# Kernel tuning notes

Hardware: AMD Instinct MI355X
Metric: run time of the kernel (lower is better)

Reference implementation:

```python
import jax, jax.numpy as jnp
import numpy as np

N, E, D, R = 50000, 600000, 128, 8


def rgcn_conv(x, ei, et, W, root, bias):
    # PyG RGCNConv with aggr='mean', root_weight=True, bias=True.
    src, dst = ei[0], ei[1]
    # per-relation transform of all node features: [N, R, D]
    xw = jnp.einsum('nd,rde->nre', x, W)
    msg = xw[src, et]                      # [E, D] gather per edge
    seg = dst * R + et                     # segment per (node, relation)
    summed = jax.ops.segment_sum(msg, seg, num_segments=N * R)
    cnt = jax.ops.segment_sum(jnp.ones((msg.shape[0],), x.dtype), seg,
                              num_segments=N * R)
    mean = summed / jnp.maximum(cnt, 1.0)[:, None]
    agg = mean.reshape(N, R, D).sum(axis=1)  # sum over relations
    return agg + x @ root + bias


def setup_inputs() -> dict:
    key = jax.random.key(0)
    ks = jax.random.split(key, 9)
    s = 1.0 / np.sqrt(D)
    x = jax.random.normal(ks[0], (N, D), jnp.float32)
    ei = jax.random.randint(ks[1], (2, E), 0, N, jnp.int32)
    et = jax.random.randint(ks[2], (E,), 0, R, jnp.int32)
    W1 = jax.random.normal(ks[3], (R, D, D), jnp.float32) * s
    root1 = jax.random.normal(ks[4], (D, D), jnp.float32) * s
    b1 = jnp.zeros((D,), jnp.float32)
    W2 = jax.random.normal(ks[5], (R, D, D), jnp.float32) * s
    root2 = jax.random.normal(ks[6], (D, D), jnp.float32) * s
    b2 = jnp.zeros((D,), jnp.float32)
    rel_emb = jax.random.normal(ks[7], (R, D), jnp.float32)
    return {"x": x, "ei": ei, "et": et, "W1": W1, "root1": root1, "b1": b1,
            "W2": W2, "root2": root2, "b2": b2, "rel_emb": rel_emb}


def reference(x, ei, et, W1, root1, b1, W2, root2, b2, rel_emb):
    h = jax.nn.relu(rgcn_conv(x, ei, et, W1, root1, b1))
    h = jax.nn.relu(rgcn_conv(h, ei, et, W2, root2, b2))
    return (h, rel_emb)
```

## Files before the change

kernel.cpp:

```cpp
#include <hip/hip_runtime.h>
#include <stdint.h>

#define N_NODES 50000
#define N_EDGES 600000
#define N_REL   8
#define KDIM    1152
#define KA      1024
#define NPAD    50048
#define RCAP    16
#define ZROW    N_NODES

typedef short v8s __attribute__((ext_vector_type(8)));
typedef float v4f __attribute__((ext_vector_type(4)));
typedef float v2f __attribute__((ext_vector_type(2)));
typedef unsigned short u16;
typedef unsigned int   u32;
typedef __attribute__((address_space(1))) const u32 gas_u32;
typedef __attribute__((address_space(3))) u32 las_u32;

__device__ __forceinline__ float bf2f(u16 u) {
    union { u32 i; float f; } t; t.i = ((u32)u) << 16; return t.f;
}
__device__ __forceinline__ u16 f2bf(float f) {
    union { float f; u32 i; } t; t.f = f;
    u32 lsb = (t.i >> 16) & 1u;
    t.i += 0x7fffu + lsb;
    return (u16)(t.i >> 16);
}
__device__ __forceinline__ v2f bfpair(u32 g) {
    union { u32 i; float f; } a, b;
    a.i = g << 16; b.i = g & 0xffff0000u;
    return (v2f){a.f, b.f};
}
__device__ __forceinline__ float load_f(const void* p, int i, int fl) {
    return fl ? bf2f(((const u16*)p)[i]) : ((const float*)p)[i];
}
__device__ __forceinline__ int wave_detect(const u32* __restrict__ x32) {
    u32 w = x32[threadIdx.x & 63];
    u32 e = (w >> 7) & 0xffu;
    unsigned long long m = __ballot(e >= 112u && e < 144u);
    return __popcll(m) >= 32;
}

#define B_CF    2344
#define B_CONV  (B_CF + 3125)
#define B_PREPW (B_CONV + 1153)
#define B_RELEMB (B_PREPW + 4)
__global__ void k_prep(const void* __restrict__ x, const int* __restrict__ ei,
                       const int* __restrict__ et,
                       const void* __restrict__ W1, const void* __restrict__ r1,
                       const void* __restrict__ b1, const void* __restrict__ W2,
                       const void* __restrict__ r2, const void* __restrict__ b2,
                       const void* __restrict__ rel_emb,
                       u16* __restrict__ xc, u16* __restrict__ Wbig,
                       u16* __restrict__ bc, int* __restrict__ cnt,
                       u16* __restrict__ evalF, void* __restrict__ out) {
    int b = blockIdx.x, tid = threadIdx.x;
    int fl = wave_detect((const u32*)x);
    if (b < B_CF) {
        int i = b * 256 + tid;
        if (i < N_EDGES) {
            int d = ei[N_EDGES + i];
            int bkt = d * N_REL + et[i];
            int pos = atomicAdd(&cnt[bkt], 1);
            if (pos < RCAP) evalF[(size_t)bkt * RCAP + pos] = (u16)ei[i];
        }
    } else if (b < B_CONV) {
        int g = (b - B_CF) * 256 + tid;
        if (fl) {
            ((int4*)xc)[g] = ((const int4*)x)[g];
        } else {
            const float* xf = (const float*)x + g * 8;
            u16 o[8];
            #pragma unroll
            for (int j = 0; j < 8; ++j) o[j] = f2bf(xf[j]);
            *(int4*)(xc + g * 8) = *(const int4*)o;
        }
    } else if (b < B_PREPW) {
        int o = (b - B_CONV) * 256 + tid;
        if (o < 2 * 128 * KDIM) {
            int l = o / (128 * KDIM);
            int rem = o - l * (128 * KDIM);
            int j = rem / KDIM, k = rem - j * KDIM;
            float v;
            if (k < 1024) {
                int r = k >> 7, kk = k & 127;
                v = load_f(l ? W2 : W1, r * 16384 + kk * 128 + j, fl);
            } else {
                v = load_f(l ? r2 : r1, (k - 1024) * 128 + j, fl);
            }
            Wbig[o] = f2bf(v);
        } else if (o < 2 * 128 * KDIM + 256) {
            int o2 = o - 2 * 128 * KDIM;
            bc[o2] = f2bf(load_f((o2 >> 7) ? b2 : b1, o2 & 127, fl));
        }
    } else {
        int i = (b - B_PREPW) * 256 + tid;
        if (i < N_REL * 128) {
            size_t o = (size_t)N_NODES * 128 + i;
            if (fl) ((u16*)out)[o]   = ((const u16*)rel_emb)[i];
            else    ((float*)out)[o] = ((const float*)rel_emb)[i];
        }
    }
}

__global__ __launch_bounds__(256) void k_agg_all(
        const u16* __restrict__ feat,
        const int* __restrict__ cnt, const u16* __restrict__ evalF,
        u16* __restrict__ aggAll) {
    int wave = threadIdx.x >> 6, lane = threadIdx.x & 63;
    int node = blockIdx.x * 4 + wave;
    if (node >= N_NODES) return;
    u32 lane4 = (u32)lane * 4u;
    int base = node * N_REL;

    int4 ca = ((const int4*)(cnt + base))[0];
    int4 cb = ((const int4*)(cnt + base))[1];
    int cs[8] = {ca.x, ca.y, ca.z, ca.w, cb.x, cb.y, cb.z, cb.w};
    const u16* eb = evalF + (size_t)base * RCAP;
    ushort4 eg[8];
    #pragma unroll
    for (int r = 0; r < N_REL; ++r)
        eg[r] = *(const ushort4*)(eb + r * RCAP);

    const char* fb = (const char*)feat;
    v2f acc[N_REL];
    #pragma unroll
    for (int r = 0; r < N_REL; ++r) {
        int c = cs[r];
        u32 o0 = ((u32)(c > 0 ? (int)eg[r].x : ZROW) << 8) + lane4;
        u32 o1 = ((u32)(c > 1 ? (int)eg[r].y : ZROW) << 8) + lane4;
        u32 o2 = ((u32)(c > 2 ? (int)eg[r].z : ZROW) << 8) + lane4;
        u32 o3 = ((u32)(c > 3 ? (int)eg[r].w : ZROW) << 8) + lane4;
        u32 g0 = *(const u32*)(fb + o0);
        u32 g1 = *(const u32*)(fb + o1);
        u32 g2 = *(const u32*)(fb + o2);
        u32 g3 = *(const u32*)(fb + o3);
        acc[r] = (bfpair(g0) + bfpair(g1)) + (bfpair(g2) + bfpair(g3));
    }

    int cmax = cs[0];
    #pragma unroll
    for (int r = 1; r < N_REL; ++r) cmax = cs[r] > cmax ? cs[r] : cmax;
    if (cmax > 4) {
        #pragma unroll
        for (int r = 0; r < N_REL; ++r) {
            int c = cs[r] < RCAP ? cs[r] : RCAP;
            for (int j = 4; j < c; ++j) {
                u32 oj = ((u32)eb[r * RCAP + j] << 8) + lane4;
                acc[r] += bfpair(*(const u32*)(fb + oj));
            }
        }
    }

    u32* d32 = (u32*)(aggAll + (size_t)node * KA) + lane;
    #pragma unroll
    for (int r = 0; r < N_REL; ++r) {
        int cc = cs[r] < RCAP ? cs[r] : RCAP;
        if (cc < 1) cc = 1;
        float inv = __builtin_amdgcn_rcpf((float)cc);
        float mx = acc[r].x * inv, my = acc[r].y * inv;
        u32 pk;
        asm("v_cvt_pk_bf16_f32 %0, %1, %2" : "=v"(pk) : "v"(mx), "v"(my));
        d32[r * 64] = pk;
    }
}

__global__ __launch_bounds__(512, 4) void k_gemm(
        const u16* __restrict__ A,
        const u16* __restrict__ feat,
        const u16* __restrict__ Bw,
        const u16* __restrict__ bias,
        const u32* __restrict__ xdet,
        u16* __restrict__ hout, void* __restrict__ fout,
        int final_out) {
    __shared__ __align__(16) u16 As[128 * 128];
    __shared__ __align__(16) u16 Bs[128 * 128];
    int tid = threadIdx.x;
    int fl = wave_detect(xdet);
    int bm0 = blockIdx.x * 128;
    int wave = tid >> 6, lane = tid & 63;
    int wm = (wave & 3) * 32, wn = (wave >> 2) * 64;
    int lrow = lane & 15, quad = lane >> 4;

    v4f accr[2][4];
    #pragma unroll
    for (int i = 0; i < 2; ++i)
        #pragma unroll
        for (int j = 0; j < 4; ++j) accr[i][j] = (v4f){0.f, 0.f, 0.f, 0.f};

    for (int h = 0; h < 9; ++h) {
        if (h) __syncthreads();
        #pragma unroll
        for (int j = 0; j < 4; ++j) {
            int off = wave * 4096 + j * 1024 + lane * 16;
            int row = off >> 8;
            int swz = (off >> 4) & 15;
            int cc = swz ^ (row & 15);
            const u16* srcA = (h < 8)
                ? A + (size_t)(bm0 + row) * KA + h * 128 + cc * 8
                : feat + (size_t)(bm0 + row) * 128 + cc * 8;
            __builtin_amdgcn_global_load_lds((gas_u32*)srcA,
                (las_u32*)(As + (off >> 1) - lane * 8), 16, 0, 0);
            __builtin_amdgcn_global_load_lds(
                (gas_u32*)(Bw + (size_t)row * KDIM + h * 128 + cc * 8),
                (las_u32*)(Bs + (off >> 1) - lane * 8), 16, 0, 0);
        }
        __syncthreads();

        #pragma unroll
        for (int kk = 0; kk < 4; ++kk) {
            int chunk = kk * 4 + quad;
            v8s a[2], b[4];
            #pragma unroll
            for (int t = 0; t < 2; ++t) {
                int row = wm + t * 16 + lrow;
                a[t] = *(const v8s*)(As + row * 128 + (chunk ^ (row & 15)) * 8);
            }
            #pragma unroll
            for (int t = 0; t < 4; ++t) {
                int row = wn + t * 16 + lrow;
                b[t] = *(const v8s*)(Bs + row * 128 + (chunk ^ (row & 15)) * 8);
            }
            #pragma unroll
            for (int ti = 0; ti < 2; ++ti)
                #pragma unroll
                for (int tj = 0; tj < 4; ++tj)
                    accr[ti][tj] = __builtin_amdgcn_mfma_f32_16x16x32_bf16(a[ti], b[tj], accr[ti][tj], 0, 0, 0);
        }
    }

    #pragma unroll
    for (int ti = 0; ti < 2; ++ti)
        #pragma unroll
        for (int reg = 0; reg < 4; ++reg) {
            int gm = bm0 + wm + ti * 16 + quad * 4 + reg;
            if (gm >= N_NODES) continue;
            #pragma unroll
            for (int tj = 0; tj < 4; ++tj) {
                int col = wn + tj * 16 + lrow;
                size_t idx = (size_t)gm * 128 + col;
                float v = fmaxf(accr[ti][tj][reg] + bf2f(bias[col]), 0.f);
                if (!final_out) hout[idx] = f2bf(v);
                else if (fl)    ((u16*)fout)[idx] = f2bf(v);
                else            ((float*)fout)[idx] = v;
            }
        }
}

static inline size_t align_up(size_t x, size_t a) { return (x + a - 1) & ~(a - 1); }

extern "C" void kernel_launch(void* const* d_in, const int* in_sizes, int n_in,
                              void* d_out, int out_size, void* d_ws, size_t ws_size,
                              hipStream_t stream) {
    const int* ei = (const int*)d_in[1];
    const int* et = (const int*)d_in[2];

    char* ws = (char*)d_ws;
    size_t off = 0;
    u16* Wbig   = (u16*)(ws + off);  off = align_up(off + (size_t)2 * 128 * KDIM * 2, 256);
    u16* bc     = (u16*)(ws + off);  off = align_up(off + 512, 256);
    u16* xc     = (u16*)(ws + off);  off = align_up(off + (size_t)NPAD * 128 * 2, 256);
    int* cnt    = (int*)(ws + off);  off = align_up(off + (size_t)N_NODES * N_REL * 4, 256);
    u16* evalF  = (u16*)(ws + off);  off = align_up(off + (size_t)N_NODES * N_REL * RCAP * 2, 256);
    u16* h      = (u16*)(ws + off);  off = align_up(off + (size_t)NPAD * 128 * 2, 256);
    u16* aggAll = (u16*)(ws + off);  off += (size_t)NPAD * KA * 2;
    (void)in_sizes; (void)n_in; (void)out_size; (void)ws_size;

    hipMemsetAsync(cnt, 0, (size_t)N_NODES * N_REL * 4, stream);
    hipMemsetAsync(xc + (size_t)ZROW * 128, 0, 256, stream);
    hipMemsetAsync(h  + (size_t)ZROW * 128, 0, 256, stream);
    k_prep<<<B_RELEMB, 256, 0, stream>>>(d_in[0], ei, et, d_in[3], d_in[4], d_in[5],
                                         d_in[6], d_in[7], d_in[8], d_in[9],
                                         xc, Wbig, bc, cnt, evalF, d_out);

    for (int l = 0; l < 2; ++l) {
        const u16* src = l ? h : xc;
        k_agg_all<<<(N_NODES + 3) / 4, 256, 0, stream>>>(src, cnt, evalF, aggAll);
        k_gemm<<<NPAD / 128, 512, 0, stream>>>(aggAll, src, Wbig + (size_t)l * 128 * KDIM,
                                               bc + l * 128, (const u32*)d_in[0],
                                               h, d_out, l);
    }
}
```

Baseline: 258.7 us.

## Reorder RGCN to transform features per relation before mean aggregation

```diff
diff --git a/kernel.cpp b/kernel.cpp
--- a/kernel.cpp
+++ b/kernel.cpp
@@ -4,11 +4,11 @@
 #define N_NODES 50000
 #define N_EDGES 600000
 #define N_REL   8
-#define KDIM    1152
-#define KA      1024
+#define NPLANE  9
 #define NPAD    50048
 #define RCAP    16
 #define ZROW    N_NODES
+#define PLSZ    (NPAD * 256u)
 
 typedef short v8s __attribute__((ext_vector_type(8)));
 typedef float v4f __attribute__((ext_vector_type(4)));
@@ -45,14 +45,15 @@
 #define B_CF    2344
 #define B_CONV  (B_CF + 3125)
 #define B_PREPW (B_CONV + 1153)
-#define B_RELEMB (B_PREPW + 4)
+#define B_RELEMB (B_PREPW + 5)
 __global__ void k_prep(const void* __restrict__ x, const int* __restrict__ ei,
                        const int* __restrict__ et,
                        const void* __restrict__ W1, const void* __restrict__ r1,
                        const void* __restrict__ b1, const void* __restrict__ W2,
                        const void* __restrict__ r2, const void* __restrict__ b2,
                        const void* __restrict__ rel_emb,
-                       u16* __restrict__ xc, u16* __restrict__ Wbig,
+                       u16* __restrict__ xc, u16* __restrict__ hbuf,
+                       u16* __restrict__ Wt,
                        u16* __restrict__ bc, int* __restrict__ cnt,
                        u16* __restrict__ evalF, void* __restrict__ out) {
     int b = blockIdx.x, tid = threadIdx.x;
@@ -78,39 +79,112 @@
         }
     } else if (b < B_PREPW) {
         int o = (b - B_CONV) * 256 + tid;
-        if (o < 2 * 128 * KDIM) {
-            int l = o / (128 * KDIM);
-            int rem = o - l * (128 * KDIM);
-            int j = rem / KDIM, k = rem - j * KDIM;
-            float v;
-            if (k < 1024) {
-                int r = k >> 7, kk = k & 127;
-                v = load_f(l ? W2 : W1, r * 16384 + kk * 128 + j, fl);
-            } else {
-                v = load_f(l ? r2 : r1, (k - 1024) * 128 + j, fl);
-            }
-            Wbig[o] = f2bf(v);
-        } else if (o < 2 * 128 * KDIM + 256) {
-            int o2 = o - 2 * 128 * KDIM;
+        if (o < 2 * NPLANE * 16384) {
+            int l = o / (NPLANE * 16384);
+            int rem = o - l * (NPLANE * 16384);
+            int rr = rem >> 14;
+            int j = (rem >> 7) & 127;
+            int k = rem & 127;
+            float v = (rr < 8)
+                ? load_f(l ? W2 : W1, rr * 16384 + k * 128 + j, fl)
+                : load_f(l ? r2 : r1, k * 128 + j, fl);
+            Wt[o] = f2bf(v);
+        } else if (o < 2 * NPLANE * 16384 + 256) {
+            int o2 = o - 2 * NPLANE * 16384;
             bc[o2] = f2bf(load_f((o2 >> 7) ? b2 : b1, o2 & 127, fl));
         }
-    } else {
+    } else if (b < B_PREPW + 4) {
         int i = (b - B_PREPW) * 256 + tid;
         if (i < N_REL * 128) {
             size_t o = (size_t)N_NODES * 128 + i;
             if (fl) ((u16*)out)[o]   = ((const u16*)rel_emb)[i];
             else    ((float*)out)[o] = ((const float*)rel_emb)[i];
         }
-    }
-}
-
-__global__ __launch_bounds__(256) void k_agg_all(
+    } else {
+        if (tid < 64)        ((u32*)(xc   + (size_t)ZROW * 128))[tid]      = 0;
+        else if (tid < 128)  ((u32*)(hbuf + (size_t)ZROW * 128))[tid - 64] = 0;
+    }
+}
+
+__global__ __launch_bounds__(512, 4) void k_gemmT(
         const u16* __restrict__ feat,
+        const u16* __restrict__ Wt,
+        u16* __restrict__ Y) {
+    __shared__ __align__(16) u16 As[128 * 128];
+    __shared__ __align__(16) u16 Bs[128 * 128];
+    int tid = threadIdx.x;
+    int bx = blockIdx.x;
+    int mb = bx / 9, rp = bx - mb * 9;
+    int bm0 = mb * 128;
+    int wave = tid >> 6, lane = tid & 63;
+    int wm = (wave & 3) * 32, wn = (wave >> 2) * 64;
+    int lrow = lane & 15, quad = lane >> 4;
+
+    v4f accr[2][4];
+    #pragma unroll
+    for (int i = 0; i < 2; ++i)
+        #pragma unroll
+        for (int j = 0; j < 4; ++j) accr[i][j] = (v4f){0.f, 0.f, 0.f, 0.f};
+
+    #pragma unroll
+    for (int j = 0; j < 4; ++j) {
+        int off = wave * 4096 + j * 1024 + lane * 16;
+        int row = off >> 8;
+        int cc = ((off >> 4) & 15) ^ (row & 15);
+        __builtin_amdgcn_global_load_lds(
+            (gas_u32*)(feat + (size_t)(bm0 + row) * 128 + cc * 8),
+            (las_u32*)(As + (off >> 1) - lane * 8), 16, 0, 0);
+        __builtin_amdgcn_global_load_lds(
+            (gas_u32*)(Wt + ((rp * 128 + row) << 7) + cc * 8),
+            (las_u32*)(Bs + (off >> 1) - lane * 8), 16, 0, 0);
+    }
+    __syncthreads();
+
+    #pragma unroll
+    for (int kk = 0; kk < 4; ++kk) {
+        int chunk = kk * 4 + quad;
+        v8s a[2], b[4];
+        #pragma unroll
+        for (int t = 0; t < 2; ++t) {
+            int row = wm + t * 16 + lrow;
+            a[t] = *(const v8s*)(As + row * 128 + (chunk ^ (row & 15)) * 8);
+        }
+        #pragma unroll
+        for (int t = 0; t < 4; ++t) {
+            int row = wn + t * 16 + lrow;
+            b[t] = *(const v8s*)(Bs + row * 128 + (chunk ^ (row & 15)) * 8);
+        }
+        #pragma unroll
+        for (int ti = 0; ti < 2; ++ti)
+            #pragma unroll
+            for (int tj = 0; tj < 4; ++tj)
+                accr[ti][tj] = __builtin_amdgcn_mfma_f32_16x16x32_bf16(a[ti], b[tj], accr[ti][tj], 0, 0, 0);
+    }
+
+    u16* yp = Y + ((size_t)rp * NPAD + bm0) * 128;
+    #pragma unroll
+    for (int ti = 0; ti < 2; ++ti)
+        #pragma unroll
+        for (int reg = 0; reg < 4; ++reg) {
+            int rloc = wm + ti * 16 + quad * 4 + reg;
+            #pragma unroll
+            for (int tj = 0; tj < 4; ++tj) {
+                int col = wn + tj * 16 + lrow;
+                yp[(size_t)rloc * 128 + col] = f2bf(accr[ti][tj][reg]);
+            }
+        }
+}
+
+__global__ __launch_bounds__(256) void k_out(
+        const u16* __restrict__ Y,
         const int* __restrict__ cnt, const u16* __restrict__ evalF,
-        u16* __restrict__ aggAll) {
+        const u16* __restrict__ bias,
+        const u32* __restrict__ xdet,
+        u16* __restrict__ hout, void* __restrict__ fout, int final_out) {
     int wave = threadIdx.x >> 6, lane = threadIdx.x & 63;
     int node = blockIdx.x * 4 + wave;
     if (node >= N_NODES) return;
+    int fl = wave_detect(xdet);
     u32 lane4 = (u32)lane * 4u;
     int base = node * N_REL;
 
@@ -123,15 +197,16 @@
     for (int r = 0; r < N_REL; ++r)
         eg[r] = *(const ushort4*)(eb + r * RCAP);
 
-    const char* fb = (const char*)feat;
+    const char* fb = (const char*)Y;
     v2f acc[N_REL];
     #pragma unroll
     for (int r = 0; r < N_REL; ++r) {
         int c = cs[r];
-        u32 o0 = ((u32)(c > 0 ? (int)eg[r].x : ZROW) << 8) + lane4;
-        u32 o1 = ((u32)(c > 1 ? (int)eg[r].y : ZROW) << 8) + lane4;
-        u32 o2 = ((u32)(c > 2 ? (int)eg[r].z : ZROW) << 8) + lane4;
-        u32 o3 = ((u32)(c > 3 ? (int)eg[r].w : ZROW) << 8) + lane4;
+        u32 pb = (u32)r * PLSZ;
+        u32 o0 = pb + ((u32)(c > 0 ? (int)eg[r].x : ZROW) << 8) + lane4;
+        u32 o1 = pb + ((u32)(c > 1 ? (int)eg[r].y : ZROW) << 8) + lane4;
+        u32 o2 = pb + ((u32)(c > 2 ? (int)eg[r].z : ZROW) << 8) + lane4;
+        u32 o3 = pb + ((u32)(c > 3 ? (int)eg[r].w : ZROW) << 8) + lane4;
         u32 g0 = *(const u32*)(fb + o0);
         u32 g1 = *(const u32*)(fb + o1);
         u32 g2 = *(const u32*)(fb + o2);
@@ -147,105 +222,36 @@
         for (int r = 0; r < N_REL; ++r) {
             int c = cs[r] < RCAP ? cs[r] : RCAP;
             for (int j = 4; j < c; ++j) {
-                u32 oj = ((u32)eb[r * RCAP + j] << 8) + lane4;
+                u32 oj = (u32)r * PLSZ + ((u32)eb[r * RCAP + j] << 8) + lane4;
                 acc[r] += bfpair(*(const u32*)(fb + oj));
             }
         }
     }
 
-    u32* d32 = (u32*)(aggAll + (size_t)node * KA) + lane;
+    v2f sum = bfpair(*(const u32*)(fb + 8u * PLSZ + ((u32)node << 8) + lane4));
+    sum += bfpair(*(const u32*)((const char*)bias + lane4));
     #pragma unroll
     for (int r = 0; r < N_REL; ++r) {
         int cc = cs[r] < RCAP ? cs[r] : RCAP;
         if (cc < 1) cc = 1;
         float inv = __builtin_amdgcn_rcpf((float)cc);
-        float mx = acc[r].x * inv, my = acc[r].y * inv;
+        sum.x += acc[r].x * inv;
+        sum.y += acc[r].y * inv;
+    }
+    float sx = fmaxf(sum.x, 0.f), sy = fmaxf(sum.y, 0.f);
+    size_t oidx = (size_t)node * 128 + lane * 2;
+    if (!final_out) {
         u32 pk;
-        asm("v_cvt_pk_bf16_f32 %0, %1, %2" : "=v"(pk) : "v"(mx), "v"(my));
-        d32[r * 64] = pk;
-    }
-}
-
-__global__ __launch_bounds__(512, 4) void k_gemm(
-        const u16* __restrict__ A,
-        const u16* __restrict__ feat,
-        const u16* __restrict__ Bw,
-        const u16* __restrict__ bias,
-        const u32* __restrict__ xdet,
-        u16* __restrict__ hout, void* __restrict__ fout,
-        int final_out) {
-    __shared__ __align__(16) u16 As[128 * 128];
-    __shared__ __align__(16) u16 Bs[128 * 128];
-    int tid = threadIdx.x;
-    int fl = wave_detect(xdet);
-    int bm0 = blockIdx.x * 128;
-    int wave = tid >> 6, lane = tid & 63;
-    int wm = (wave & 3) * 32, wn = (wave >> 2) * 64;
-    int lrow = lane & 15, quad = lane >> 4;
-
-    v4f accr[2][4];
-    #pragma unroll
-    for (int i = 0; i < 2; ++i)
-        #pragma unroll
-        for (int j = 0; j < 4; ++j) accr[i][j] = (v4f){0.f, 0.f, 0.f, 0.f};
-
-    for (int h = 0; h < 9; ++h) {
-        if (h) __syncthreads();
-        #pragma unroll
-        for (int j = 0; j < 4; ++j) {
-            int off = wave * 4096 + j * 1024 + lane * 16;
-            int row = off >> 8;
-            int swz = (off >> 4) & 15;
-            int cc = swz ^ (row & 15);
-            const u16* srcA = (h < 8)
-                ? A + (size_t)(bm0 + row) * KA + h * 128 + cc * 8
-                : feat + (size_t)(bm0 + row) * 128 + cc * 8;
-            __builtin_amdgcn_global_load_lds((gas_u32*)srcA,
-                (las_u32*)(As + (off >> 1) - lane * 8), 16, 0, 0);
-            __builtin_amdgcn_global_load_lds(
-                (gas_u32*)(Bw + (size_t)row * KDIM + h * 128 + cc * 8),
-                (las_u32*)(Bs + (off >> 1) - lane * 8), 16, 0, 0);
-        }
-        __syncthreads();
-
-        #pragma unroll
-        for (int kk = 0; kk < 4; ++kk) {
-            int chunk = kk * 4 + quad;
-            v8s a[2], b[4];
-            #pragma unroll
-            for (int t = 0; t < 2; ++t) {
-                int row = wm + t * 16 + lrow;
-                a[t] = *(const v8s*)(As + row * 128 + (chunk ^ (row & 15)) * 8);
-            }
-            #pragma unroll
-            for (int t = 0; t < 4; ++t) {
-                int row = wn + t * 16 + lrow;
-                b[t] = *(const v8s*)(Bs + row * 128 + (chunk ^ (row & 15)) * 8);
-            }
-            #pragma unroll
-            for (int ti = 0; ti < 2; ++ti)
-                #pragma unroll
-                for (int tj = 0; tj < 4; ++tj)
-                    accr[ti][tj] = __builtin_amdgcn_mfma_f32_16x16x32_bf16(a[ti], b[tj], accr[ti][tj], 0, 0, 0);
-        }
-    }
-
-    #pragma unroll
-    for (int ti = 0; ti < 2; ++ti)
-        #pragma unroll
-        for (int reg = 0; reg < 4; ++reg) {
-            int gm = bm0 + wm + ti * 16 + quad * 4 + reg;
-            if (gm >= N_NODES) continue;
-            #pragma unroll
-            for (int tj = 0; tj < 4; ++tj) {
-                int col = wn + tj * 16 + lrow;
-                size_t idx = (size_t)gm * 128 + col;
-                float v = fmaxf(accr[ti][tj][reg] + bf2f(bias[col]), 0.f);
-                if (!final_out) hout[idx] = f2bf(v);
-                else if (fl)    ((u16*)fout)[idx] = f2bf(v);
-                else            ((float*)fout)[idx] = v;
-            }
-        }
+        asm("v_cvt_pk_bf16_f32 %0, %1, %2" : "=v"(pk) : "v"(sx), "v"(sy));
+        *(u32*)(hout + oidx) = pk;
+    } else if (fl) {
+        u32 pk;
+        asm("v_cvt_pk_bf16_f32 %0, %1, %2" : "=v"(pk) : "v"(sx), "v"(sy));
+        *(u32*)((u16*)fout + oidx) = pk;
+    } else {
+        ((float*)fout)[oidx]     = sx;
+        ((float*)fout)[oidx + 1] = sy;
+    }
 }
 
 static inline size_t align_up(size_t x, size_t a) { return (x + a - 1) & ~(a - 1); }
@@ -258,27 +264,24 @@
 
     char* ws = (char*)d_ws;
     size_t off = 0;
-    u16* Wbig   = (u16*)(ws + off);  off = align_up(off + (size_t)2 * 128 * KDIM * 2, 256);
+    u16* Wt     = (u16*)(ws + off);  off = align_up(off + (size_t)2 * NPLANE * 16384 * 2, 256);
     u16* bc     = (u16*)(ws + off);  off = align_up(off + 512, 256);
     u16* xc     = (u16*)(ws + off);  off = align_up(off + (size_t)NPAD * 128 * 2, 256);
     int* cnt    = (int*)(ws + off);  off = align_up(off + (size_t)N_NODES * N_REL * 4, 256);
     u16* evalF  = (u16*)(ws + off);  off = align_up(off + (size_t)N_NODES * N_REL * RCAP * 2, 256);
     u16* h      = (u16*)(ws + off);  off = align_up(off + (size_t)NPAD * 128 * 2, 256);
-    u16* aggAll = (u16*)(ws + off);  off += (size_t)NPAD * KA * 2;
+    u16* Y      = (u16*)(ws + off);  off += (size_t)NPLANE * NPAD * 128 * 2;
     (void)in_sizes; (void)n_in; (void)out_size; (void)ws_size;
 
     hipMemsetAsync(cnt, 0, (size_t)N_NODES * N_REL * 4, stream);
-    hipMemsetAsync(xc + (size_t)ZROW * 128, 0, 256, stream);
-    hipMemsetAsync(h  + (size_t)ZROW * 128, 0, 256, stream);
     k_prep<<<B_RELEMB, 256, 0, stream>>>(d_in[0], ei, et, d_in[3], d_in[4], d_in[5],
                                          d_in[6], d_in[7], d_in[8], d_in[9],
-                                         xc, Wbig, bc, cnt, evalF, d_out);
+                                         xc, h, Wt, bc, cnt, evalF, d_out);
 
     for (int l = 0; l < 2; ++l) {
         const u16* src = l ? h : xc;
-        k_agg_all<<<(N_NODES + 3) / 4, 256, 0, stream>>>(src, cnt, evalF, aggAll);
-        k_gemm<<<NPAD / 128, 512, 0, stream>>>(aggAll, src, Wbig + (size_t)l * 128 * KDIM,
-                                               bc + l * 128, (const u32*)d_in[0],
-                                               h, d_out, l);
-    }
-}
+        k_gemmT<<<(NPAD / 128) * 9, 512, 0, stream>>>(src, Wt + (size_t)l * NPLANE * 16384, Y);
+        k_out<<<(N_NODES + 3) / 4, 256, 0, stream>>>(Y, cnt, evalF, bc + l * 128,
+                                                     (const u32*)d_in[0], h, d_out, l);
+    }
+}
```

New measurement: 263.5 us. About the same (+1.9%).
